# Kernel optimization log

Hardware: AMD Instinct MI355X
Metric: run time of the kernel (lower is better)

## Reference

```python
import jax, jax.numpy as jnp
import numpy as np

D_MODEL = 2048
HEADDIM = 32
NHEADS = D_MODEL // HEADDIM  # 64
BLOCK = 256
EPS = 1e-4


def segsum(x):
    # x: (..., T) -> (..., T, T) stable segment sums, -inf above diagonal
    T = x.shape[-1]
    xe = jnp.broadcast_to(x[..., None], x.shape + (T,))  # (..., d, e)
    lower = jnp.tril(jnp.ones((T, T), dtype=bool), -1)
    xe = jnp.where(lower, xe, 0.0)
    s = jnp.cumsum(xe, axis=-2)
    incl = jnp.tril(jnp.ones((T, T), dtype=bool), 0)
    return jnp.where(incl, s, -jnp.inf)


def ssd_minimal_discrete(X, A, B, C, block_len):
    # X: (b, L, h, p); A: (b, L, h); B, C: (b, L, h, n). L % block_len == 0.
    b, Lm, h, p = X.shape
    c = Lm // block_len
    Xb = X.reshape(b, c, block_len, h, p)
    Bb = B.reshape(b, c, block_len, h, B.shape[-1])
    Cb = C.reshape(b, c, block_len, h, C.shape[-1])
    Ab = A.reshape(b, c, block_len, h).transpose(0, 3, 1, 2)  # (b, h, c, l)
    A_cumsum = jnp.cumsum(Ab, axis=-1)
    Lmat = jnp.exp(segsum(Ab))  # (b, h, c, l, s)
    # 1. intra-chunk (diagonal block) output
    Y_diag = jnp.einsum('bclhn,bcshn,bhcls,bcshp->bclhp', Cb, Bb, Lmat, Xb)
    # 2. per-chunk states
    decay_states = jnp.exp(A_cumsum[:, :, :, -1:] - A_cumsum)  # (b, h, c, l)
    states = jnp.einsum('bclhn,bhcl,bclhp->bchpn', Bb, decay_states, Xb)
    # 3. inter-chunk recurrence
    init = jnp.zeros_like(states[:, :1])
    states = jnp.concatenate([init, states], axis=1)  # (b, c+1, h, p, n)
    A_last = jnp.pad(A_cumsum[:, :, :, -1], ((0, 0), (0, 0), (1, 0)))  # (b, h, c+1)
    decay_chunk = jnp.exp(segsum(A_last))  # (b, h, c+1, c+1)
    new_states = jnp.einsum('bhzc,bchpn->bzhpn', decay_chunk, states)
    states_in, final_state = new_states[:, :-1], new_states[:, -1]
    # 4. state -> output within chunks
    state_decay_out = jnp.exp(A_cumsum)  # (b, h, c, l)
    Y_off = jnp.einsum('bclhn,bchpn,bhcl->bclhp', Cb, states_in, state_decay_out)
    Y = (Y_diag + Y_off).reshape(b, Lm, h, p)
    return Y, final_state


def setup_inputs() -> dict:
    key = jax.random.key(0)
    k1, k2 = jax.random.split(key)
    Bsz, Lfull, M = 2, 4096, 2048
    hidden_states = jax.random.normal(k1, (Bsz, M, D_MODEL), dtype=jnp.float32)
    # boundaries at even positions: exactly M boundaries per row, position 0 is a boundary
    boundary_mask = jnp.broadcast_to((jnp.arange(Lfull) % 2 == 0)[None, :], (Bsz, Lfull))
    boundary_prob = jax.random.uniform(k2, (Bsz, Lfull, 2), dtype=jnp.float32)
    mask = jnp.ones((Bsz, Lfull), dtype=bool)
    return {"hidden_states": hidden_states, "boundary_mask": boundary_mask,
            "boundary_prob": boundary_prob, "mask": mask}


def reference(hidden_states, boundary_mask, boundary_prob, mask):
    Bsz, Lfull = boundary_mask.shape
    M = hidden_states.shape[1]
    # select boundary-position probabilities, in order, first M
    p = jnp.clip(boundary_prob[..., -1].astype(jnp.float32), EPS, 1.0 - EPS)
    token_idx = jnp.arange(Lfull)[None, :] + (~boundary_mask).astype(jnp.int32) * Lfull
    order = jnp.argsort(token_idx, axis=1, stable=True)
    p_sel = jnp.take_along_axis(p, order[:, :M], axis=1)  # (B, M)
    dt = jnp.log(1.0 / (1.0 - p_sel))
    x = hidden_states.astype(jnp.float32) / dt[..., None]
    Xr = x.reshape(Bsz, M, NHEADS, HEADDIM)
    A_dt = -jnp.broadcast_to(dt[:, :, None], (Bsz, M, NHEADS))  # A = -1, A*dt
    B_ssd = jnp.broadcast_to(p_sel[:, :, None, None], (Bsz, M, NHEADS, 1))
    C_ssd = jnp.ones_like(B_ssd)
    out, _ = ssd_minimal_discrete(Xr, A_dt, B_ssd, C_ssd, BLOCK)
    out = out.reshape(Bsz, M, D_MODEL)
    # plug back: each uncompressed token reads the EMA value of its chunk
    plug = jnp.cumsum(boundary_mask.astype(jnp.int32), axis=1) - 1  # (B, L)
    out = jnp.take_along_axis(out, plug[:, :, None], axis=1)  # (B, L, d_model)
    return out
```

## Files before the change

### kernel.cpp

```cpp
#include <hip/hip_runtime.h>
#include <math.h>

#define BSZ    2
#define LFULL  4096
#define MLEN   2048
#define DMODEL 2048
#define CLIP_EPS 1e-4f
#define CCH    256
#define TCH    8

typedef float f4 __attribute__((ext_vector_type(4)));

__global__ __launch_bounds__(256) void k1_prep(
    const int* __restrict__ bmask_raw, const float* __restrict__ bprob,
    int* __restrict__ Ls, int* __restrict__ Le,
    float* __restrict__ wA, float* __restrict__ eA,
    float* __restrict__ cde, float* __restrict__ Pc)
{
  const int b   = blockIdx.x;
  const int tid = threadIdx.x;

  __shared__ int   s_cnt[257];
  __shared__ int   s_mode;
  __shared__ int   s_ntrue;
  __shared__ int   s_sel[MLEN];
  __shared__ float s_e[MLEN];

  if (tid == 0) {
    unsigned w0 = ((const unsigned*)bmask_raw)[0];
    s_mode = (w0 <= 1u) ? 1 : 0;
  }
  __syncthreads();
  const int mode = s_mode;
  const unsigned char* bmask_u8 = (const unsigned char*)bmask_raw;

  const int PER = LFULL / 256;
  const int base = tid * PER;

  int cnt = 0;
  for (int i = 0; i < PER; ++i) {
    const int L = base + i;
    const int v = mode ? (bmask_raw[b * LFULL + L] != 0)
                       : (bmask_u8[b * LFULL + L] != 0);
    cnt += v;
  }
  s_cnt[tid] = cnt;
  __syncthreads();
  if (tid == 0) {
    int acc = 0;
    for (int i = 0; i < 256; ++i) { int c = s_cnt[i]; s_cnt[i] = acc; acc += c; }
    s_cnt[256] = acc;
    s_ntrue = acc;
  }
  __syncthreads();
  const int ntrue = s_ntrue;

  int trun = s_cnt[tid];
  for (int i = 0; i < PER; ++i) {
    const int L = base + i;
    const int v = mode ? (bmask_raw[b * LFULL + L] != 0)
                       : (bmask_u8[b * LFULL + L] != 0);
    if (v) {
      if (trun < MLEN) s_sel[trun] = L;
      ++trun;
    } else {
      const int f = L - trun;
      const int slot = ntrue + f;
      if (slot < MLEN) s_sel[slot] = L;
    }
  }
  __syncthreads();

  for (int j = tid; j < MLEN; j += 256) {
    const int L = s_sel[j];
    float p = bprob[((size_t)b * LFULL + L) * 2 + 1];
    p = fminf(fmaxf(p, CLIP_EPS), 1.0f - CLIP_EPS);
    const float dt = -log1pf(-p);
    wA[b * MLEN + j] = p / dt;
    const float e = 1.0f - p;
    eA[b * MLEN + j] = e;
    s_e[j] = e;
  }
  __syncthreads();

  {
    const int c = tid;
    const int o = c * TCH;
    float run = 1.0f;
    #pragma unroll
    for (int i = 0; i < TCH; ++i) {
      run *= s_e[o + i];
      cde[b * MLEN + o + i] = run;
    }
    Pc[b * CCH + c] = run;
  }

  const int nb = (ntrue < MLEN) ? ntrue : MLEN;
  for (int j = tid; j < MLEN; j += 256) {
    int ls, le;
    if (nb == 0) {
      ls = (j == 0) ? 0 : LFULL;
      le = (j == 0) ? LFULL : LFULL;
    } else if (j < nb) {
      ls = (j == 0) ? 0 : s_sel[j];
      le = (j == nb - 1) ? LFULL : s_sel[j + 1];
    } else {
      ls = LFULL; le = LFULL;
    }
    Ls[b * MLEN + j] = ls;
    Le[b * MLEN + j] = le;
  }
}

__global__ __launch_bounds__(256) void k2_states(
    const float* __restrict__ hid, const float* __restrict__ wA,
    const float* __restrict__ eA, float* __restrict__ S)
{
  const int tid = threadIdx.x;
  const int c = blockIdx.y;
  const int b = blockIdx.z;

  __shared__ float s_w[TCH], s_e[TCH];
  if (tid < TCH)            s_w[tid]       = wA[b * MLEN + c * TCH + tid];
  else if (tid < 2 * TCH)   s_e[tid - TCH] = eA[b * MLEN + c * TCH + (tid - TCH)];
  __syncthreads();

  const int d4 = blockIdx.x * 256 + tid;
  const f4* xp = (const f4*)hid + ((size_t)(b * MLEN + c * TCH) * DMODEL >> 2) + d4;

  f4 st = {0.f, 0.f, 0.f, 0.f};
  #pragma unroll
  for (int t = 0; t < TCH; ++t) {
    const f4 x = xp[(size_t)t * (DMODEL / 4)];
    const float w = s_w[t], e = s_e[t];
    st.x = fmaf(e, st.x, w * x.x);
    st.y = fmaf(e, st.y, w * x.y);
    st.z = fmaf(e, st.z, w * x.z);
    st.w = fmaf(e, st.w, w * x.w);
  }
  ((f4*)S)[((size_t)(b * CCH + c) * DMODEL >> 2) + d4] = st;
}

__global__ __launch_bounds__(256) void k25_scan(
    const float* __restrict__ Pc, float* __restrict__ S)
{
  const int c  = threadIdx.x;
  const int d4 = blockIdx.x;
  const int b  = blockIdx.y;

  __shared__ float sP[CCH];
  __shared__ f4    sS[CCH];

  f4* Sf4 = (f4*)S;
  const size_t idx = ((size_t)(b * CCH + c) * DMODEL >> 2) + d4;

  sP[c] = Pc[b * CCH + c];
  sS[c] = Sf4[idx];
  __syncthreads();

  #pragma unroll
  for (int dstep = 1; dstep < CCH; dstep <<= 1) {
    float pd = 1.0f;
    f4 sd = {0.f, 0.f, 0.f, 0.f};
    if (c >= dstep) { pd = sP[c - dstep]; sd = sS[c - dstep]; }
    __syncthreads();
    if (c >= dstep) {
      f4 cur = sS[c];
      const float pc = sP[c];
      cur.x = fmaf(pc, sd.x, cur.x);
      cur.y = fmaf(pc, sd.y, cur.y);
      cur.z = fmaf(pc, sd.z, cur.z);
      cur.w = fmaf(pc, sd.w, cur.w);
      sS[c] = cur;
      sP[c] = pc * pd;
    }
    __syncthreads();
  }

  f4 g = {0.f, 0.f, 0.f, 0.f};
  if (c > 0) g = sS[c - 1];
  Sf4[idx] = g;
}

__global__ __launch_bounds__(256) void k3_out(
    const float* __restrict__ hid, const float* __restrict__ wA,
    const float* __restrict__ eA, const float* __restrict__ cde,
    const float* __restrict__ G,
    const int* __restrict__ Ls, const int* __restrict__ Le,
    float* __restrict__ out)
{
  const int tid = threadIdx.x;
  const int c = blockIdx.y;
  const int b = blockIdx.z;

  __shared__ float s_w[TCH], s_e[TCH], s_c[TCH];
  __shared__ int   s_ls[TCH], s_le[TCH];
  const int o = b * MLEN + c * TCH;
  if (tid < TCH)          { s_w[tid] = wA[o + tid];  s_ls[tid] = Ls[o + tid]; }
  else if (tid < 2 * TCH) { const int t = tid - TCH;     s_e[t] = eA[o + t]; s_le[t] = Le[o + t]; }
  else if (tid < 3 * TCH) { const int t = tid - 2 * TCH; s_c[t] = cde[o + t]; }
  __syncthreads();

  const int d4 = blockIdx.x * 256 + tid;

  const f4 H = ((const f4*)G)[((size_t)(b * CCH + c) * DMODEL >> 2) + d4];

  const f4* xp = (const f4*)hid + ((size_t)(b * MLEN + c * TCH) * DMODEL >> 2) + d4;
  f4*       op = (f4*)out + ((size_t)b * LFULL * DMODEL >> 2) + d4;

  f4 st = {0.f, 0.f, 0.f, 0.f};
  #pragma unroll
  for (int t = 0; t < TCH; ++t) {
    const f4 x = xp[(size_t)t * (DMODEL / 4)];
    const float w = s_w[t], e = s_e[t], cd = s_c[t];
    st.x = fmaf(e, st.x, w * x.x);
    st.y = fmaf(e, st.y, w * x.y);
    st.z = fmaf(e, st.z, w * x.z);
    st.w = fmaf(e, st.w, w * x.w);
    f4 y;
    y.x = fmaf(cd, H.x, st.x);
    y.y = fmaf(cd, H.y, st.y);
    y.z = fmaf(cd, H.z, st.z);
    y.w = fmaf(cd, H.w, st.w);
    const int ls = s_ls[t], le = s_le[t];
    for (int L = ls; L < le; ++L) {
      __builtin_nontemporal_store(y, op + (size_t)L * (DMODEL / 4));
    }
  }
}

extern "C" void kernel_launch(void* const* d_in, const int* in_sizes, int n_in,
                              void* d_out, int out_size, void* d_ws, size_t ws_size,
                              hipStream_t stream) {
  const float* hid   = (const float*)d_in[0];
  const int*   bmask = (const int*)d_in[1];
  const float* bprob = (const float*)d_in[2];
  float*       out   = (float*)d_out;

  char* ws = (char*)d_ws;
  const size_t SZI = (size_t)BSZ * MLEN * sizeof(int);
  const size_t SZF = (size_t)BSZ * MLEN * sizeof(float);
  int*   Ls  = (int*)(ws);
  int*   Le  = (int*)(ws + SZI);
  float* wA  = (float*)(ws + 2 * SZI);
  float* eA  = (float*)(ws + 2 * SZI + SZF);
  float* cde = (float*)(ws + 2 * SZI + 2 * SZF);
  float* Pc  = (float*)(ws + 2 * SZI + 3 * SZF);
  float* S   = (float*)(ws + 2 * SZI + 3 * SZF + 4096);

  k1_prep<<<dim3(BSZ), dim3(256), 0, stream>>>(bmask, bprob, Ls, Le, wA, eA, cde, Pc);

  dim3 grid(DMODEL / 1024, CCH, BSZ);
  k2_states<<<grid, dim3(256), 0, stream>>>(hid, wA, eA, S);

  k25_scan<<<dim3(DMODEL / 4, BSZ), dim3(256), 0, stream>>>(Pc, S);

  k3_out<<<grid, dim3(256), 0, stream>>>(hid, wA, eA, cde, S, Ls, Le, out);
}
```

Measured before the change: 129.6 us.

## Fuse state, scan and output kernels into one cooperative kernel with grid syncs

Replaces the three kernels for chunk states, the cross-chunk scan and the output with a single cooperative kernel of 1024 blocks that uses grid.sync between phases. Each block keeps its per-timestep local states in shared memory, so the output phase no longer re-reads the hidden states or recomputes the recurrence. This saves two launches and one full read of the input. In exchange it needs all 1024 blocks resident at once (about 40KB of shared memory per block, launch bounds raised for occupancy) and pays the cost of two grid-wide barriers.

New measurement: 335.0 us. 2.58x slower.

```diff
diff --git a/kernel.cpp b/kernel.cpp
--- a/kernel.cpp
+++ b/kernel.cpp
@@ -1,5 +1,8 @@
 #include <hip/hip_runtime.h>
+#include <hip/hip_cooperative_groups.h>
 #include <math.h>
+
+namespace cg = cooperative_groups;
 
 #define BSZ    2
 #define LFULL  4096
@@ -8,6 +11,7 @@
 #define CLIP_EPS 1e-4f
 #define CCH    256
 #define TCH    8
+#define NBLK   (BSZ * CCH * 2)
 
 typedef float f4 __attribute__((ext_vector_type(4)));
 
@@ -112,119 +116,104 @@
   }
 }
 
-__global__ __launch_bounds__(256) void k2_states(
-    const float* __restrict__ hid, const float* __restrict__ wA,
-    const float* __restrict__ eA, float* __restrict__ S)
-{
-  const int tid = threadIdx.x;
-  const int c = blockIdx.y;
-  const int b = blockIdx.z;
-
-  __shared__ float s_w[TCH], s_e[TCH];
-  if (tid < TCH)            s_w[tid]       = wA[b * MLEN + c * TCH + tid];
-  else if (tid < 2 * TCH)   s_e[tid - TCH] = eA[b * MLEN + c * TCH + (tid - TCH)];
-  __syncthreads();
-
-  const int d4 = blockIdx.x * 256 + tid;
-  const f4* xp = (const f4*)hid + ((size_t)(b * MLEN + c * TCH) * DMODEL >> 2) + d4;
-
-  f4 st = {0.f, 0.f, 0.f, 0.f};
-  #pragma unroll
-  for (int t = 0; t < TCH; ++t) {
-    const f4 x = xp[(size_t)t * (DMODEL / 4)];
-    const float w = s_w[t], e = s_e[t];
-    st.x = fmaf(e, st.x, w * x.x);
-    st.y = fmaf(e, st.y, w * x.y);
-    st.z = fmaf(e, st.z, w * x.z);
-    st.w = fmaf(e, st.w, w * x.w);
-  }
-  ((f4*)S)[((size_t)(b * CCH + c) * DMODEL >> 2) + d4] = st;
-}
-
-__global__ __launch_bounds__(256) void k25_scan(
-    const float* __restrict__ Pc, float* __restrict__ S)
-{
-  const int c  = threadIdx.x;
-  const int d4 = blockIdx.x;
-  const int b  = blockIdx.y;
-
-  __shared__ float sP[CCH];
-  __shared__ f4    sS[CCH];
-
-  f4* Sf4 = (f4*)S;
-  const size_t idx = ((size_t)(b * CCH + c) * DMODEL >> 2) + d4;
-
-  sP[c] = Pc[b * CCH + c];
-  sS[c] = Sf4[idx];
-  __syncthreads();
-
-  #pragma unroll
-  for (int dstep = 1; dstep < CCH; dstep <<= 1) {
-    float pd = 1.0f;
-    f4 sd = {0.f, 0.f, 0.f, 0.f};
-    if (c >= dstep) { pd = sP[c - dstep]; sd = sS[c - dstep]; }
-    __syncthreads();
-    if (c >= dstep) {
-      f4 cur = sS[c];
-      const float pc = sP[c];
-      cur.x = fmaf(pc, sd.x, cur.x);
-      cur.y = fmaf(pc, sd.y, cur.y);
-      cur.z = fmaf(pc, sd.z, cur.z);
-      cur.w = fmaf(pc, sd.w, cur.w);
-      sS[c] = cur;
-      sP[c] = pc * pd;
-    }
-    __syncthreads();
-  }
-
-  f4 g = {0.f, 0.f, 0.f, 0.f};
-  if (c > 0) g = sS[c - 1];
-  Sf4[idx] = g;
-}
-
-__global__ __launch_bounds__(256) void k3_out(
+__global__ __launch_bounds__(256, 4) void k_fused(
     const float* __restrict__ hid, const float* __restrict__ wA,
     const float* __restrict__ eA, const float* __restrict__ cde,
-    const float* __restrict__ G,
-    const int* __restrict__ Ls, const int* __restrict__ Le,
-    float* __restrict__ out)
+    const float* __restrict__ Pc, const int* __restrict__ Ls,
+    const int* __restrict__ Le, float* __restrict__ S,
+    float* __restrict__ G, float* __restrict__ out)
 {
+  cg::grid_group grid = cg::this_grid();
+  const int lid = blockIdx.x;
   const int tid = threadIdx.x;
-  const int c = blockIdx.y;
-  const int b = blockIdx.z;
-
+
+  __shared__ f4    s_yloc[TCH * 256];
+  __shared__ float s_scanP[CCH];
+  __shared__ f4    s_scanS[CCH];
   __shared__ float s_w[TCH], s_e[TCH], s_c[TCH];
   __shared__ int   s_ls[TCH], s_le[TCH];
-  const int o = b * MLEN + c * TCH;
-  if (tid < TCH)          { s_w[tid] = wA[o + tid];  s_ls[tid] = Ls[o + tid]; }
-  else if (tid < 2 * TCH) { const int t = tid - TCH;     s_e[t] = eA[o + t]; s_le[t] = Le[o + t]; }
-  else if (tid < 3 * TCH) { const int t = tid - 2 * TCH; s_c[t] = cde[o + t]; }
-  __syncthreads();
-
-  const int d4 = blockIdx.x * 256 + tid;
-
-  const f4 H = ((const f4*)G)[((size_t)(b * CCH + c) * DMODEL >> 2) + d4];
-
-  const f4* xp = (const f4*)hid + ((size_t)(b * MLEN + c * TCH) * DMODEL >> 2) + d4;
-  f4*       op = (f4*)out + ((size_t)b * LFULL * DMODEL >> 2) + d4;
-
-  f4 st = {0.f, 0.f, 0.f, 0.f};
-  #pragma unroll
-  for (int t = 0; t < TCH; ++t) {
-    const f4 x = xp[(size_t)t * (DMODEL / 4)];
-    const float w = s_w[t], e = s_e[t], cd = s_c[t];
-    st.x = fmaf(e, st.x, w * x.x);
-    st.y = fmaf(e, st.y, w * x.y);
-    st.z = fmaf(e, st.z, w * x.z);
-    st.w = fmaf(e, st.w, w * x.w);
-    f4 y;
-    y.x = fmaf(cd, H.x, st.x);
-    y.y = fmaf(cd, H.y, st.y);
-    y.z = fmaf(cd, H.z, st.z);
-    y.w = fmaf(cd, H.w, st.w);
-    const int ls = s_ls[t], le = s_le[t];
-    for (int L = ls; L < le; ++L) {
-      __builtin_nontemporal_store(y, op + (size_t)L * (DMODEL / 4));
+
+  const int xA = lid & 1;
+  const int cA = (lid >> 1) & (CCH - 1);
+  const int bA = lid >> 9;
+  const int d4 = xA * 256 + tid;
+
+  {
+    const int o = bA * MLEN + cA * TCH;
+    if (tid < TCH)          { s_w[tid] = wA[o + tid];  s_ls[tid] = Ls[o + tid]; }
+    else if (tid < 2 * TCH) { const int t = tid - TCH;     s_e[t] = eA[o + t]; s_le[t] = Le[o + t]; }
+    else if (tid < 3 * TCH) { const int t = tid - 2 * TCH; s_c[t] = cde[o + t]; }
+  }
+  __syncthreads();
+
+  {
+    const f4* xp = (const f4*)hid + ((size_t)(bA * MLEN + cA * TCH) * DMODEL >> 2) + d4;
+    f4 st = {0.f, 0.f, 0.f, 0.f};
+    #pragma unroll
+    for (int t = 0; t < TCH; ++t) {
+      const f4 xv = xp[(size_t)t * (DMODEL / 4)];
+      const float w = s_w[t], e = s_e[t];
+      st.x = fmaf(e, st.x, w * xv.x);
+      st.y = fmaf(e, st.y, w * xv.y);
+      st.z = fmaf(e, st.z, w * xv.z);
+      st.w = fmaf(e, st.w, w * xv.w);
+      s_yloc[t * 256 + tid] = st;
+    }
+    ((f4*)S)[((size_t)(bA * CCH + cA) * DMODEL >> 2) + d4] = st;
+  }
+
+  grid.sync();
+
+  {
+    const int d4b = lid & 511;
+    const int bb  = lid >> 9;
+    const int c   = tid;
+    s_scanP[c] = Pc[bb * CCH + c];
+    s_scanS[c] = ((const f4*)S)[((size_t)(bb * CCH + c) * DMODEL >> 2) + d4b];
+    __syncthreads();
+
+    #pragma unroll
+    for (int dstep = 1; dstep < CCH; dstep <<= 1) {
+      float pd = 1.0f;
+      f4 sd = {0.f, 0.f, 0.f, 0.f};
+      if (c >= dstep) { pd = s_scanP[c - dstep]; sd = s_scanS[c - dstep]; }
+      __syncthreads();
+      if (c >= dstep) {
+        f4 cur = s_scanS[c];
+        const float pc = s_scanP[c];
+        cur.x = fmaf(pc, sd.x, cur.x);
+        cur.y = fmaf(pc, sd.y, cur.y);
+        cur.z = fmaf(pc, sd.z, cur.z);
+        cur.w = fmaf(pc, sd.w, cur.w);
+        s_scanS[c] = cur;
+        s_scanP[c] = pc * pd;
+      }
+      __syncthreads();
+    }
+
+    f4 g = {0.f, 0.f, 0.f, 0.f};
+    if (c > 0) g = s_scanS[c - 1];
+    ((f4*)G)[((size_t)(bb * CCH + c) * DMODEL >> 2) + d4b] = g;
+  }
+
+  grid.sync();
+
+  {
+    const f4 H = ((const f4*)G)[((size_t)(bA * CCH + cA) * DMODEL >> 2) + d4];
+    f4* op = (f4*)out + ((size_t)bA * LFULL * DMODEL >> 2) + d4;
+    #pragma unroll
+    for (int t = 0; t < TCH; ++t) {
+      const f4 st = s_yloc[t * 256 + tid];
+      const float cd = s_c[t];
+      f4 y;
+      y.x = fmaf(cd, H.x, st.x);
+      y.y = fmaf(cd, H.y, st.y);
+      y.z = fmaf(cd, H.z, st.z);
+      y.w = fmaf(cd, H.w, st.w);
+      const int ls = s_ls[t], le = s_le[t];
+      for (int L = ls; L < le; ++L) {
+        __builtin_nontemporal_store(y, op + (size_t)L * (DMODEL / 4));
+      }
     }
   }
 }
@@ -247,13 +236,12 @@
   float* cde = (float*)(ws + 2 * SZI + 2 * SZF);
   float* Pc  = (float*)(ws + 2 * SZI + 3 * SZF);
   float* S   = (float*)(ws + 2 * SZI + 3 * SZF + 4096);
+  float* G   = (float*)(ws + 2 * SZI + 3 * SZF + 4096 + (size_t)4 * 1024 * 1024);
 
   k1_prep<<<dim3(BSZ), dim3(256), 0, stream>>>(bmask, bprob, Ls, Le, wA, eA, cde, Pc);
 
-  dim3 grid(DMODEL / 1024, CCH, BSZ);
-  k2_states<<<grid, dim3(256), 0, stream>>>(hid, wA, eA, S);
-
-  k25_scan<<<dim3(DMODEL / 4, BSZ), dim3(256), 0, stream>>>(Pc, S);
-
-  k3_out<<<grid, dim3(256), 0, stream>>>(hid, wA, eA, cde, S, Ls, Le, out);
+  void* args[] = { (void*)&hid, (void*)&wA, (void*)&eA, (void*)&cde, (void*)&Pc,
+                   (void*)&Ls, (void*)&Le, (void*)&S, (void*)&G, (void*)&out };
+  hipLaunchCooperativeKernel((const void*)k_fused, dim3(NBLK), dim3(256),
+                             args, 0, stream);
 }
```
